# Performance work log

Measured on AMD Instinct MI355X. Metric: run time of the kernel, lower is better.

The kernel has to match this reference:

```python
import jax, jax.numpy as jnp
import numpy as np

# Mamba3/SSD selective state-space mixer (scalar-A-per-head SSD recurrence,
# causal depthwise conv on x/B/C, gated RMSNorm, in/out projections).
D_MODEL = 1024
EXPAND = 2
D_INNER = EXPAND * D_MODEL            # 2048
HEADDIM = D_MODEL // 16               # 64  (head_count=16 -> headdim 64)
NHEADS = D_INNER // HEADDIM           # 32
D_STATE = 128
CONV_W = 4
CONV_DIM = D_INNER + 2 * D_STATE      # x, B, C share the conv
D_IN_PROJ = 2 * D_INNER + 2 * D_STATE + NHEADS  # z, x, B, C, dt
EPS = 1e-5


def setup_inputs() -> dict:
    key = jax.random.key(0)
    ks = jax.random.split(key, 8)
    B, L = 4, 2048
    hidden = jax.random.normal(ks[0], (B, L, D_MODEL), dtype=jnp.float32)
    W_in = jax.random.normal(ks[1], (D_MODEL, D_IN_PROJ), dtype=jnp.float32) * 0.02
    conv_w = jax.random.normal(ks[2], (CONV_DIM, CONV_W), dtype=jnp.float32) * 0.2
    conv_b = jnp.zeros((CONV_DIM,), dtype=jnp.float32)
    # dt_bias: inverse-softplus of dt ~ U[1e-3, 0.1]
    dt = jnp.exp(jax.random.uniform(ks[3], (NHEADS,)) * (np.log(0.1) - np.log(1e-3)) + np.log(1e-3))
    dt_bias = dt + jnp.log(-jnp.expm1(-dt))
    A_log = jnp.log(jax.random.uniform(ks[4], (NHEADS,), minval=1.0, maxval=16.0))
    D = jnp.ones((NHEADS,), dtype=jnp.float32)
    norm_w = jnp.ones((D_INNER,), dtype=jnp.float32)
    W_out = jax.random.normal(ks[5], (D_INNER, D_MODEL), dtype=jnp.float32) * 0.02
    return {"hidden": hidden, "W_in": W_in, "conv_w": conv_w, "conv_b": conv_b,
            "dt_bias": dt_bias, "A_log": A_log, "D": D, "norm_w": norm_w, "W_out": W_out}


def _silu(x):
    return x * jax.nn.sigmoid(x)


def _mixer(hidden, W_in, conv_w, conv_b, dt_bias, A_log, D, norm_w, W_out):
    Bsz, L, _ = hidden.shape
    zxbcdt = hidden @ W_in                                    # [B,L,D_IN_PROJ]
    z = zxbcdt[..., :D_INNER]
    xBC = zxbcdt[..., D_INNER:D_INNER + CONV_DIM]
    dt = zxbcdt[..., -NHEADS:]                                # [B,L,H]
    # causal depthwise conv, width 4 (small fixed loop over taps)
    xp = jnp.pad(xBC, ((0, 0), (CONV_W - 1, 0), (0, 0)))
    conv = sum(xp[:, k:k + L, :] * conv_w[:, k] for k in range(CONV_W))
    xBC = _silu(conv + conv_b)
    x = xBC[..., :D_INNER].reshape(Bsz, L, NHEADS, HEADDIM)   # [B,L,H,P]
    Bm = xBC[..., D_INNER:D_INNER + D_STATE]                  # [B,L,N]
    Cm = xBC[..., D_INNER + D_STATE:]                         # [B,L,N]
    dt = jax.nn.softplus(dt + dt_bias)                        # [B,L,H]
    dA = jnp.exp(dt * (-jnp.exp(A_log)))                      # [B,L,H] decay in (0,1)
    dBx = jnp.einsum('blh,bln,blhp->blhpn', dt, Bm, x)        # [B,L,H,P,N]

    def step(h, inp):
        dA_t, dBx_t, C_t = inp                                # [B,H],[B,H,P,N],[B,N]
        h = dA_t[:, :, None, None] * h + dBx_t
        y = jnp.einsum('bhpn,bn->bhp', h, C_t)
        return h, y

    h0 = jnp.zeros((Bsz, NHEADS, HEADDIM, D_STATE), dtype=hidden.dtype)
    xs = (jnp.moveaxis(dA, 1, 0), jnp.moveaxis(dBx, 1, 0), jnp.moveaxis(Cm, 1, 0))
    _, ys = jax.lax.scan(step, h0, xs)                        # [L,B,H,P]
    y = jnp.moveaxis(ys, 0, 1) + D[None, None, :, None] * x   # skip term
    y = y.reshape(Bsz, L, D_INNER)
    # gated RMSNorm: norm(y * silu(z))
    y = y * _silu(z)
    y = y * jax.lax.rsqrt(jnp.mean(y * y, axis=-1, keepdims=True) + EPS) * norm_w
    return y @ W_out


def reference(hidden, W_in, conv_w, conv_b, dt_bias, A_log, D, norm_w, W_out):
    return _mixer(hidden, W_in, conv_w, conv_b, dt_bias, A_log, D, norm_w, W_out)
```

## Files before the change

### kernel.cpp

```cpp
#include <hip/hip_runtime.h>
#include <math.h>

#define BSZ 4
#define LEN 2048
#define DM 1024
#define DI 2048
#define HD 64
#define NH 32
#define DS 128
#define CD 2304
#define DP 4384
#define NTOK (BSZ*LEN)
#define QCH 128
#define NCH (LEN/QCH)
#define TOFF (DP-NH)

#define CONV_R 64
#define NRB (NTOK/CONV_R)
#define NPAD 4352

typedef unsigned short ushort_t;
typedef __bf16 bf16x8 __attribute__((ext_vector_type(8)));
typedef ushort_t us8 __attribute__((ext_vector_type(8)));
typedef float f32x4 __attribute__((ext_vector_type(4)));

__device__ __forceinline__ ushort_t f2bf(float f) {
    unsigned u = __float_as_uint(f);
    unsigned r = (u + 0x7FFFu + ((u >> 16) & 1u)) >> 16;
    return (ushort_t)r;
}
__device__ __forceinline__ float bf2f(ushort_t u) {
    return __uint_as_float(((unsigned)u) << 16);
}
__device__ __forceinline__ bf16x8 us2bf(us8 v) {
    union { us8 u; bf16x8 b; } x; x.u = v; return x.b;
}

__device__ __forceinline__ void gl_lds16(const void* g, void* l) {
    __builtin_amdgcn_global_load_lds(
        (const __attribute__((address_space(1))) void*)g,
        (__attribute__((address_space(3))) void*)l, 16, 0, 0);
}

__global__ __launch_bounds__(256) void cvt_bf16(
    const float* __restrict__ A, ushort_t* __restrict__ Ab)
{
    size_t i = ((size_t)blockIdx.x * 256 + threadIdx.x) * 4;
    float4 v = *(const float4*)(A + i);
    ushort_t o[4] = { f2bf(v.x), f2bf(v.y), f2bf(v.z), f2bf(v.w) };
    *(uint2*)(Ab + i) = *(uint2*)o;
}

__global__ __launch_bounds__(256) void transpose_cvt(
    const float* __restrict__ W, ushort_t* __restrict__ Wt,
    const float* __restrict__ colscale, int K, int N, int ldw)
{
    __shared__ float T[32][33];
    const int n0 = blockIdx.x * 32;
    const int k0 = blockIdx.y * 32;
    const int tid = threadIdx.x;
    #pragma unroll
    for (int l = 0; l < 4; l++) {
        int idx = tid + l * 256;
        int ki = idx >> 5, nj = idx & 31;
        int n = n0 + nj;
        float s = colscale ? colscale[k0 + ki] : 1.f;
        T[ki][nj] = (n < N) ? W[(size_t)(k0 + ki) * ldw + n] * s : 0.f;
    }
    __syncthreads();
    #pragma unroll
    for (int l = 0; l < 4; l++) {
        int idx = tid + l * 256;
        int nj = idx >> 5, ki = idx & 31;
        Wt[(size_t)(n0 + nj) * K + k0 + ki] = f2bf(T[ki][nj]);
    }
}

template <bool OB>
__global__ __launch_bounds__(256) void gemm128(
    const ushort_t* __restrict__ A, const ushort_t* __restrict__ Bt,
    void* __restrict__ Cp, const float* __restrict__ rowscale,
    int K, int lda, int ldb, int ldc)
{
    __shared__ __align__(16) ushort_t LA[2][128 * 64];
    __shared__ __align__(16) ushort_t LB[2][128 * 64];
    const int tid = threadIdx.x;
    int bid = blockIdx.y * gridDim.x + blockIdx.x;
    const int nwg = gridDim.x * gridDim.y;
    if (!(nwg & 7)) bid = (bid & 7) * (nwg >> 3) + (bid >> 3);
    const int n0 = (bid % gridDim.x) * 128;
    const int m0 = (bid / gridDim.x) * 128;
    const int lane = tid & 63;
    const int w = tid >> 6;
    const int wm = w >> 1, wn = w & 1;
    const int lm = lane & 15, quad = lane >> 4;
    const int swz = (lm & 7) << 4;
    const int ck0 = ((0 * 64 + quad * 16) ^ swz) >> 1;
    const int ck1 = ((1 * 64 + quad * 16) ^ swz) >> 1;

    const int srow = tid >> 3;
    const int scolb = ((tid & 7) * 16) ^ ((srow & 7) << 4);
    const char* gA = (const char*)A + ((size_t)(m0 + srow) * lda) * 2 + scolb;
    const char* gB = (const char*)Bt + ((size_t)(n0 + srow) * ldb) * 2 + scolb;
    const size_t strA = (size_t)32 * lda * 2;
    const size_t strB = (size_t)32 * ldb * 2;
    const int ldst = tid * 8;

    f32x4 acc[4][4];
    #pragma unroll
    for (int i = 0; i < 4; i++)
        #pragma unroll
        for (int j = 0; j < 4; j++) acc[i][j] = (f32x4){0.f, 0.f, 0.f, 0.f};

    const int NTt = K >> 6;

    auto STAGE = [&](int kt1, int nxt) {
        const char* a = gA + (size_t)kt1 * 128;
        const char* b = gB + (size_t)kt1 * 128;
        #pragma unroll
        for (int j = 0; j < 4; j++)
            gl_lds16(a + j * strA, &LA[nxt][j * 2048 + ldst]);
        #pragma unroll
        for (int j = 0; j < 4; j++)
            gl_lds16(b + j * strB, &LB[nxt][j * 2048 + ldst]);
    };

    STAGE(0, 0);

    for (int kt = 0; kt < NTt; ++kt) {
        const int cur = kt & 1;
        __builtin_amdgcn_s_barrier();
        if (kt + 1 < NTt) {
            STAGE(kt + 1, cur ^ 1);
            asm volatile("s_waitcnt vmcnt(8)" ::: "memory");
        } else {
            asm volatile("s_waitcnt vmcnt(0)" ::: "memory");
        }
        __builtin_amdgcn_s_barrier();

        bf16x8 af[4][2], bf[4][2];
        #pragma unroll
        for (int s = 0; s < 4; s++) {
            const int rb = (wm * 64 + s * 16 + lm) << 6;
            af[s][0] = *(const bf16x8*)&LA[cur][rb + ck0];
            af[s][1] = *(const bf16x8*)&LA[cur][rb + ck1];
        }
        #pragma unroll
        for (int t = 0; t < 4; t++) {
            const int rb = (wn * 64 + t * 16 + lm) << 6;
            bf[t][0] = *(const bf16x8*)&LB[cur][rb + ck0];
            bf[t][1] = *(const bf16x8*)&LB[cur][rb + ck1];
        }
        __builtin_amdgcn_s_setprio(1);
        #pragma unroll
        for (int kk = 0; kk < 2; kk++)
            #pragma unroll
            for (int s = 0; s < 4; s++)
                #pragma unroll
                for (int t = 0; t < 4; t++)
                    acc[s][t] = __builtin_amdgcn_mfma_f32_16x16x32_bf16(
                        af[s][kk], bf[t][kk], acc[s][t], 0, 0, 0);
        __builtin_amdgcn_s_setprio(0);
    }

    #pragma unroll
    for (int s = 0; s < 4; s++) {
        const int row = m0 + wm * 64 + s * 16 + quad * 4;
        float rs[4] = {1.f, 1.f, 1.f, 1.f};
        if (!OB && rowscale) {
            #pragma unroll
            for (int r = 0; r < 4; r++) rs[r] = rowscale[row + r];
        }
        #pragma unroll
        for (int t = 0; t < 4; t++) {
            const int col = n0 + wn * 64 + t * 16 + lm;
            #pragma unroll
            for (int r = 0; r < 4; r++) {
                if (OB)
                    ((ushort_t*)Cp)[(size_t)(row + r) * ldc + col] = f2bf(acc[s][t][r]);
                else
                    ((float*)Cp)[(size_t)(row + r) * ldc + col] = acc[s][t][r] * rs[r];
            }
        }
    }
}

__global__ __launch_bounds__(256) void conv_silu_bf16(
    const ushort_t* __restrict__ xbcb, const float* __restrict__ cw,
    const float* __restrict__ cb, ushort_t* __restrict__ xT,
    ushort_t* __restrict__ Bn, ushort_t* __restrict__ BT,
    ushort_t* __restrict__ Cn)
{
    __shared__ ushort_t Tl[256][68];
    const int tid = threadIdx.x;
    const int c = blockIdx.x * 256 + tid;
    const int rb = blockIdx.y;
    const int row0 = rb * CONV_R;
    const bool isBC = (blockIdx.x == 8);

    const float w0 = cw[c*4+0], w1 = cw[c*4+1], w2 = cw[c*4+2], w3 = cw[c*4+3];
    const float bias = cb[c];
    float h0 = 0.f, h1 = 0.f, h2 = 0.f;
    if ((row0 & (LEN - 1)) != 0) {
        h0 = bf2f(xbcb[(size_t)(row0 - 3) * NPAD + c]);
        h1 = bf2f(xbcb[(size_t)(row0 - 2) * NPAD + c]);
        h2 = bf2f(xbcb[(size_t)(row0 - 1) * NPAD + c]);
    }
    const ushort_t* p = xbcb + (size_t)row0 * NPAD + c;
    for (int r = 0; r < CONV_R; r++) {
        float xin = bf2f(*p);
        float a = bias + w0*h0 + w1*h1 + w2*h2 + w3*xin;
        ushort_t bv = f2bf(a / (1.f + __expf(-a)));
        Tl[tid][r] = bv;
        if (isBC) {
            int row = row0 + r;
            if (tid < DS) Bn[(size_t)row * DS + tid] = bv;
            else          Cn[(size_t)row * DS + (tid - DS)] = bv;
        }
        h0 = h1; h1 = h2; h2 = xin;
        p += NPAD;
    }
    __syncthreads();

    const int seg = tid & 7;
    const int clb = tid >> 3;
    if (!isBC) {
        #pragma unroll
        for (int pass = 0; pass < 8; pass++) {
            int cl = pass * 32 + clb;
            int cc = blockIdx.x * 256 + cl;
            us8 v;
            #pragma unroll
            for (int j = 0; j < 8; j++) v[j] = Tl[cl][seg * 8 + j];
            *(us8*)&xT[(size_t)cc * NTOK + row0 + seg * 8] = v;
        }
    } else {
        #pragma unroll
        for (int pass = 0; pass < 4; pass++) {
            int n = pass * 32 + clb;
            us8 v;
            #pragma unroll
            for (int j = 0; j < 8; j++) v[j] = Tl[n][seg * 8 + j];
            *(us8*)&BT[(size_t)n * NTOK + row0 + seg * 8] = v;
        }
    }
}

__global__ __launch_bounds__(256) void gct_gemm(
    const ushort_t* __restrict__ Bn, const ushort_t* __restrict__ Cn,
    float* __restrict__ Graw)
{
    const int bc = blockIdx.x;
    const int chunk = bc % NCH;
    const int b = bc / NCH;
    const size_t rowbase = (size_t)b * LEN + (size_t)chunk * QCH;
    const int tid = threadIdx.x;
    const int w = tid >> 6, lane = tid & 63;
    const int lm = lane & 15, quad = lane >> 4;
    const int tw0 = w * 32;

    f32x4 acc[2][8];
    #pragma unroll
    for (int ti = 0; ti < 2; ti++)
        #pragma unroll
        for (int sj = 0; sj < 8; sj++) acc[ti][sj] = (f32x4){0.f, 0.f, 0.f, 0.f};

    #pragma unroll
    for (int ks = 0; ks < 4; ks++) {
        const int k0 = ks * 32 + quad * 8;
        bf16x8 a0 = *(const bf16x8*)&Cn[(rowbase + tw0 + lm) * DS + k0];
        bf16x8 a1 = *(const bf16x8*)&Cn[(rowbase + tw0 + 16 + lm) * DS + k0];
        #pragma unroll
        for (int sj = 0; sj < 8; sj++) {
            bf16x8 bb = *(const bf16x8*)&Bn[(rowbase + sj * 16 + lm) * DS + k0];
            acc[0][sj] = __builtin_amdgcn_mfma_f32_16x16x32_bf16(a0, bb, acc[0][sj], 0, 0, 0);
            acc[1][sj] = __builtin_amdgcn_mfma_f32_16x16x32_bf16(a1, bb, acc[1][sj], 0, 0, 0);
        }
    }
    float* G = Graw + (size_t)bc * (QCH * QCH);
    #pragma unroll
    for (int ti = 0; ti < 2; ti++)
        #pragma unroll
        for (int sj = 0; sj < 8; sj++)
            #pragma unroll
            for (int r = 0; r < 4; r++)
                G[(size_t)(tw0 + ti * 16 + quad * 4 + r) * QCH + sj * 16 + lm] = acc[ti][sj][r];
}

__global__ __launch_bounds__(256) void dt_proc_fp32(
    const float* __restrict__ hidden, const float* __restrict__ W_in,
    const float* __restrict__ dt_bias, const float* __restrict__ A_log,
    float* __restrict__ dtv, float* __restrict__ ldA)
{
    const int h = threadIdx.x & 31;
    const int tt = threadIdx.x >> 5;
    const int t = blockIdx.x * 8 + tt;
    const float* hr = hidden + (size_t)t * DM;
    const float* wc = W_in + TOFF + h;
    float a0 = 0.f, a1 = 0.f, a2 = 0.f, a3 = 0.f;
    for (int k = 0; k < DM; k += 4) {
        a0 += hr[k+0] * wc[(size_t)(k+0) * DP];
        a1 += hr[k+1] * wc[(size_t)(k+1) * DP];
        a2 += hr[k+2] * wc[(size_t)(k+2) * DP];
        a3 += hr[k+3] * wc[(size_t)(k+3) * DP];
    }
    float v = (a0 + a1) + (a2 + a3) + dt_bias[h];
    float sp = (v > 20.f) ? v : log1pf(expf(v));
    int idx = t * NH + h;
    dtv[idx] = sp;
    ldA[idx] = -sp * expf(A_log[h]);
}

__global__ __launch_bounds__(64) void scan_chunk(
    const float* __restrict__ dtv, const float* __restrict__ ldA,
    float* __restrict__ lcpb, float* __restrict__ dtsb,
    float* __restrict__ coefb, float* __restrict__ csum)
{
    const int blk = blockIdx.x;
    const int chunk = blk % NCH;
    const int bh = blk / NCH;
    const int h = bh % NH;
    const int b = bh / NH;
    const int lane = threadIdx.x;
    const size_t rowbase = (size_t)b * LEN + (size_t)chunk * QCH;
    const int t0 = 2 * lane, t1 = 2 * lane + 1;
    float v0 = ldA[(rowbase + t0) * NH + h];
    float v1 = ldA[(rowbase + t1) * NH + h];
    float d0 = dtv[(rowbase + t0) * NH + h];
    float d1 = dtv[(rowbase + t1) * NH + h];
    float pair = v0 + v1;
    #pragma unroll
    for (int off = 1; off < 64; off <<= 1) {
        float n = __shfl_up(pair, off, 64);
        if (lane >= off) pair += n;
    }
    float l1 = pair, l0 = pair - v1;
    float total = __shfl(pair, 63, 64);
    size_t base = (size_t)blk * QCH;
    *(float2*)&lcpb[base + t0] = make_float2(l0, l1);
    *(float2*)&dtsb[base + t0] = make_float2(d0, d1);
    *(float2*)&coefb[base + t0] =
        make_float2(__expf(total - l0) * d0, __expf(total - l1) * d1);
    if (lane == 63) csum[blk] = total;
}

__global__ __launch_bounds__(256) void phase1_mfma(
    const ushort_t* __restrict__ xT, const ushort_t* __restrict__ BT,
    const float* __restrict__ coefb, float* __restrict__ S)
{
    const int h = blockIdx.x & (NH - 1);
    const int bc = blockIdx.x >> 5;
    const int chunk = bc % NCH;
    const int b = bc / NCH;
    const int blko = (b * NH + h) * NCH + chunk;
    const int tid = threadIdx.x;
    const size_t rowbase = (size_t)b * LEN + (size_t)chunk * QCH;

    __shared__ float coef[QCH];
    if (tid < QCH) coef[tid] = coefb[(size_t)blko * QCH + tid];
    __syncthreads();

    const int w = tid >> 6, lane = tid & 63;
    const int lm = lane & 15, quad = lane >> 4;
    const int nw0 = w * 32;

    f32x4 acc[4][2];
    #pragma unroll
    for (int i = 0; i < 4; i++)
        #pragma unroll
        for (int j = 0; j < 2; j++) acc[i][j] = (f32x4){0.f, 0.f, 0.f, 0.f};

    #pragma unroll
    for (int ks = 0; ks < 4; ks++) {
        const int k0 = ks * 32 + quad * 8;
        bf16x8 a[4];
        #pragma unroll
        for (int mi = 0; mi < 4; mi++)
            a[mi] = *(const bf16x8*)&xT[(size_t)(h * HD + mi * 16 + lm) * NTOK + rowbase + k0];
        float cf[8];
        #pragma unroll
        for (int j = 0; j < 8; j++) cf[j] = coef[k0 + j];
        #pragma unroll
        for (int ni = 0; ni < 2; ni++) {
            us8 raw = *(const us8*)&BT[(size_t)(nw0 + ni * 16 + lm) * NTOK + rowbase + k0];
            us8 sb;
            #pragma unroll
            for (int j = 0; j < 8; j++) sb[j] = f2bf(bf2f(raw[j]) * cf[j]);
            bf16x8 bfr = us2bf(sb);
            __builtin_amdgcn_s_setprio(1);
            #pragma unroll
            for (int mi = 0; mi < 4; mi++)
                acc[mi][ni] = __builtin_amdgcn_mfma_f32_16x16x32_bf16(a[mi], bfr, acc[mi][ni], 0, 0, 0);
            __builtin_amdgcn_s_setprio(0);
        }
    }
    float* Sb = S + (size_t)blko * (HD * DS);
    #pragma unroll
    for (int mi = 0; mi < 4; mi++)
        #pragma unroll
        for (int ni = 0; ni < 2; ni++)
            #pragma unroll
            for (int r = 0; r < 4; r++)
                Sb[(size_t)(mi * 16 + quad * 4 + r) * DS + nw0 + ni * 16 + lm] = acc[mi][ni][r];
}

__global__ __launch_bounds__(256) void phase2(
    const float* __restrict__ S, const float* __restrict__ csum,
    ushort_t* __restrict__ hsb)
{
    const int bh = blockIdx.x >> 3;
    const int esl = blockIdx.x & 7;
    const int tid = threadIdx.x;
    const int eb = esl * 1024 + tid;
    float run[4] = {0.f, 0.f, 0.f, 0.f};
    for (int c = 0; c < NCH; c++) {
        float P = __expf(csum[bh * NCH + c]);
        size_t base = (size_t)(bh * NCH + c) * (HD * DS);
        #pragma unroll
        for (int i = 0; i < 4; i++) {
            size_t idx = base + eb + i * 256;
            float s = S[idx];
            hsb[idx] = f2bf(run[i]);
            run[i] = P * run[i] + s;
        }
    }
}

__global__ __launch_bounds__(256) void phase3_mfma(
    const ushort_t* __restrict__ xT, const ushort_t* __restrict__ Cn,
    const ushort_t* __restrict__ hsb, const float* __restrict__ Graw,
    const float* __restrict__ lcpb, const float* __restrict__ dtsb,
    const float* __restrict__ Dvec, ushort_t* __restrict__ zxb,
    float* __restrict__ ss)
{
    const int tid = threadIdx.x;
    const int h = blockIdx.x & (NH - 1);
    const int bc = blockIdx.x >> 5;
    const int chunk = bc % NCH;
    const int b = bc / NCH;
    const int blko = (b * NH + h) * NCH + chunk;
    const size_t rowbase = (size_t)b * LEN + (size_t)chunk * QCH;

    __shared__ float lcp[QCH];
    __shared__ float dts[QCH];
    if (tid < QCH) {
        lcp[tid] = lcpb[(size_t)blko * QCH + tid];
        dts[tid] = dtsb[(size_t)blko * QCH + tid];
    }
    __syncthreads();

    const int w = tid >> 6, lane = tid & 63;
    const int lm = lane & 15, quad = lane >> 4;
    const int tw0 = w * 32;

    const float* Gr = Graw + (size_t)bc * (QCH * QCH);
    const ushort_t* hsp = hsb + (size_t)blko * (HD * DS);

    f32x4 acc2[2][4];
    #pragma unroll
    for (int ti = 0; ti < 2; ti++)
        #pragma unroll
        for (int pi = 0; pi < 4; pi++) acc2[ti][pi] = (f32x4){0.f, 0.f, 0.f, 0.f};

    #pragma unroll
    for (int ks = 0; ks < 8; ks++) {
        bf16x8 a[2], bb[4];
        if (ks < 4) {
            const int k0 = ks * 32 + quad * 8;
            #pragma unroll
            for (int ti = 0; ti < 2; ti++) {
                int t = tw0 + ti * 16 + lm;
                float lt = lcp[t];
                const float* gp = Gr + (size_t)t * QCH + k0;
                float4 g0 = *(const float4*)gp;
                float4 g1 = *(const float4*)(gp + 4);
                float ge[8] = { g0.x, g0.y, g0.z, g0.w, g1.x, g1.y, g1.z, g1.w };
                us8 sb;
                #pragma unroll
                for (int j = 0; j < 8; j++) {
                    int s = k0 + j;
                    float wv = (s <= t) ? (__expf(lt - lcp[s]) * dts[s]) : 0.f;
                    sb[j] = f2bf(ge[j] * wv);
                }
                a[ti] = us2bf(sb);
            }
            #pragma unroll
            for (int pi = 0; pi < 4; pi++)
                bb[pi] = *(const bf16x8*)&xT[(size_t)(h * HD + pi * 16 + lm) * NTOK + rowbase + k0];
        } else {
            const int k0 = (ks - 4) * 32 + quad * 8;
            #pragma unroll
            for (int ti = 0; ti < 2; ti++) {
                int t = tw0 + ti * 16 + lm;
                float sc = __expf(lcp[t]);
                us8 raw = *(const us8*)&Cn[(rowbase + t) * DS + k0];
                us8 sb;
                #pragma unroll
                for (int j = 0; j < 8; j++) sb[j] = f2bf(bf2f(raw[j]) * sc);
                a[ti] = us2bf(sb);
            }
            #pragma unroll
            for (int pi = 0; pi < 4; pi++)
                bb[pi] = *(const bf16x8*)&hsp[(size_t)(pi * 16 + lm) * DS + k0];
        }
        __builtin_amdgcn_s_setprio(1);
        #pragma unroll
        for (int ti = 0; ti < 2; ti++)
            #pragma unroll
            for (int pi = 0; pi < 4; pi++)
                acc2[ti][pi] = __builtin_amdgcn_mfma_f32_16x16x32_bf16(a[ti], bb[pi], acc2[ti][pi], 0, 0, 0);
        __builtin_amdgcn_s_setprio(0);
    }

    const float Dh = Dvec[h];
    float vsq[2][4] = {};
    #pragma unroll
    for (int ti = 0; ti < 2; ti++)
        #pragma unroll
        for (int pi = 0; pi < 4; pi++) {
            int tb = tw0 + ti * 16 + quad * 4;
            int col = h * HD + pi * 16 + lm;
            ushort4 xv = *(const ushort4*)&xT[(size_t)(h * HD + pi * 16 + lm) * NTOK + rowbase + tb];
            const ushort_t* xe = (const ushort_t*)&xv;
            #pragma unroll
            for (int r = 0; r < 4; r++) {
                size_t grow = rowbase + tb + r;
                float y = acc2[ti][pi][r] + Dh * bf2f(xe[r]);
                float z = bf2f(zxb[grow * NPAD + col]);
                float v = y * (z / (1.f + __expf(-z)));
                vsq[ti][r] += v * v;
                zxb[grow * NPAD + DI + col] = f2bf(v);
            }
        }
    #pragma unroll
    for (int ti = 0; ti < 2; ti++)
        #pragma unroll
        for (int r = 0; r < 4; r++) {
            float s = vsq[ti][r];
            s += __shfl_xor(s, 1, 64);
            s += __shfl_xor(s, 2, 64);
            s += __shfl_xor(s, 4, 64);
            s += __shfl_xor(s, 8, 64);
            if (lm == 0) {
                int tb = tw0 + ti * 16 + quad * 4 + r;
                atomicAdd(&ss[rowbase + tb], s);
            }
        }
}

__global__ __launch_bounds__(256) void rms_finalize(
    const float* __restrict__ ss, float* __restrict__ rr)
{
    int t = blockIdx.x * 256 + threadIdx.x;
    rr[t] = rsqrtf(ss[t] * (1.f / DI) + 1e-5f);
}

extern "C" void kernel_launch(void* const* d_in, const int* in_sizes, int n_in,
                              void* d_out, int out_size, void* d_ws, size_t ws_size,
                              hipStream_t stream)
{
    const float* hidden  = (const float*)d_in[0];
    const float* W_in    = (const float*)d_in[1];
    const float* conv_w  = (const float*)d_in[2];
    const float* conv_b  = (const float*)d_in[3];
    const float* dt_bias = (const float*)d_in[4];
    const float* A_log   = (const float*)d_in[5];
    const float* Dv      = (const float*)d_in[6];
    const float* norm_w  = (const float*)d_in[7];
    const float* W_out   = (const float*)d_in[8];
    float* out = (float*)d_out;

    char* ws = (char*)d_ws;
    size_t o = 0;
    ushort_t* zxb  = (ushort_t*)(ws + o); o += (size_t)NTOK * NPAD * 2;
    float* S       = (float*)(ws + o);    o += (size_t)BSZ * NH * NCH * HD * DS * 4;
    ushort_t* xT   = (ushort_t*)(ws + o); o += (size_t)DI * NTOK * 2;
    ushort_t* Bn   = (ushort_t*)(ws + o); o += (size_t)NTOK * DS * 2;
    ushort_t* BT   = (ushort_t*)(ws + o); o += (size_t)DS * NTOK * 2;
    ushort_t* Cn   = (ushort_t*)(ws + o); o += (size_t)NTOK * DS * 2;
    ushort_t* hsb  = (ushort_t*)(ws + o); o += (size_t)BSZ * NH * NCH * HD * DS * 2;
    float* Graw    = (float*)(ws + o);    o += (size_t)BSZ * NCH * QCH * QCH * 4;
    float* dtv     = (float*)(ws + o);    o += (size_t)NTOK * NH * 4;
    float* ldA     = (float*)(ws + o);    o += (size_t)NTOK * NH * 4;
    float* lcpb    = (float*)(ws + o);    o += (size_t)BSZ * NH * LEN * 4;
    float* dtsb    = (float*)(ws + o);    o += (size_t)BSZ * NH * LEN * 4;
    float* coefb   = (float*)(ws + o);    o += (size_t)BSZ * NH * LEN * 4;
    float* csum    = (float*)(ws + o);    o += (size_t)BSZ * NH * NCH * 4;
    float* ss      = (float*)(ws + o);    o += (size_t)NTOK * 4;
    float* rr      = (float*)(ws + o);    o += (size_t)NTOK * 4;
    ushort_t* Ah   = (ushort_t*)S;
    ushort_t* W1t  = (ushort_t*)((char*)S + (size_t)NTOK * DM * 2);
    ushort_t* Wot  = hsb;
    ushort_t* xbcb = zxb + DI;
    ushort_t* ynb  = zxb + DI;

    hipMemsetAsync(ss, 0, (size_t)NTOK * 4, stream);
    cvt_bf16<<<(NTOK * DM) / 1024, 256, 0, stream>>>(hidden, Ah);
    transpose_cvt<<<dim3(NPAD / 32, DM / 32), 256, 0, stream>>>(
        W_in, W1t, nullptr, DM, NPAD, DP);
    gemm128<true><<<dim3(NPAD / 128, NTOK / 128), 256, 0, stream>>>(
        Ah, W1t, zxb, nullptr, DM, DM, DM, NPAD);
    conv_silu_bf16<<<dim3(CD / 256, NRB), 256, 0, stream>>>(
        xbcb, conv_w, conv_b, xT, Bn, BT, Cn);
    gct_gemm<<<BSZ * NCH, 256, 0, stream>>>(Bn, Cn, Graw);
    dt_proc_fp32<<<NTOK / 8, 256, 0, stream>>>(hidden, W_in, dt_bias, A_log, dtv, ldA);
    scan_chunk<<<BSZ * NH * NCH, 64, 0, stream>>>(dtv, ldA, lcpb, dtsb, coefb, csum);
    phase1_mfma<<<BSZ * NH * NCH, 256, 0, stream>>>(xT, BT, coefb, S);
    phase2<<<BSZ * NH * 8, 256, 0, stream>>>(S, csum, hsb);
    phase3_mfma<<<BSZ * NH * NCH, 256, 0, stream>>>(
        xT, Cn, hsb, Graw, lcpb, dtsb, Dv, zxb, ss);
    rms_finalize<<<NTOK / 256, 256, 0, stream>>>(ss, rr);
    transpose_cvt<<<dim3(DM / 32, DI / 32), 256, 0, stream>>>(
        W_out, Wot, norm_w, DI, DM, DM);
    gemm128<false><<<dim3(DM / 128, NTOK / 128), 256, 0, stream>>>(
        ynb, Wot, out, rr, DI, NPAD, DI, DM);
}
```

Before: 507.2 us.

## Use triple-buffered K=32 GEMM for input projection and fold RMS finalize into output GEMM

Adds a new input-projection GEMM kernel that stages K tiles of 32 into three LDS buffers, prefetching two tiles ahead with explicit vmcnt waits. Its smaller LDS footprint lets launch bounds request three workgroups per CU, aiming for better latency hiding and occupancy. Separately, the rms_finalize kernel is dropped and the rsqrt is computed in the output GEMM epilogue directly from the sum-of-squares buffer, removing one launch and one small buffer. The trade-off is more barriers per K step and a slightly heavier epilogue.

```diff
diff --git a/kernel.cpp b/kernel.cpp
--- a/kernel.cpp
+++ b/kernel.cpp
@@ -73,6 +73,100 @@
         int idx = tid + l * 256;
         int nj = idx >> 5, ki = idx & 31;
         Wt[(size_t)(n0 + nj) * K + k0 + ki] = f2bf(T[ki][nj]);
+    }
+}
+
+__global__ __launch_bounds__(256, 3) void gemm1_tb(
+    const ushort_t* __restrict__ A, const ushort_t* __restrict__ Bt,
+    ushort_t* __restrict__ C, int K, int lda, int ldb, int ldc)
+{
+    __shared__ __align__(16) ushort_t LA[3][128 * 32];
+    __shared__ __align__(16) ushort_t LB[3][128 * 32];
+    const int tid = threadIdx.x;
+    int bid = blockIdx.y * gridDim.x + blockIdx.x;
+    const int nwg = gridDim.x * gridDim.y;
+    if (!(nwg & 7)) bid = (bid & 7) * (nwg >> 3) + (bid >> 3);
+    const int n0 = (bid % gridDim.x) * 128;
+    const int m0 = (bid / gridDim.x) * 128;
+    const int lane = tid & 63;
+    const int w = tid >> 6;
+    const int wm = w >> 1, wn = w & 1;
+    const int lm = lane & 15, quad = lane >> 4;
+    const int ck = ((quad * 16) ^ (((lm >> 1) & 3) << 4)) >> 1;
+
+    const int srow = tid >> 2;
+    const int scolb = ((tid & 3) * 16) ^ (((tid >> 3) & 3) << 4);
+    const char* gA = (const char*)A + ((size_t)(m0 + srow) * lda) * 2 + scolb;
+    const char* gB = (const char*)Bt + ((size_t)(n0 + srow) * ldb) * 2 + scolb;
+    const size_t strA = (size_t)64 * lda * 2;
+    const size_t strB = (size_t)64 * ldb * 2;
+    const int ldst = tid * 8;
+
+    f32x4 acc[4][4];
+    #pragma unroll
+    for (int i = 0; i < 4; i++)
+        #pragma unroll
+        for (int j = 0; j < 4; j++) acc[i][j] = (f32x4){0.f, 0.f, 0.f, 0.f};
+
+    const int NTt = K >> 5;
+
+    auto STAGE = [&](int kt1, int buf) {
+        const char* a = gA + (size_t)kt1 * 64;
+        const char* b = gB + (size_t)kt1 * 64;
+        gl_lds16(a + 0 * strA, &LA[buf][0 * 2048 + ldst]);
+        gl_lds16(a + 1 * strA, &LA[buf][1 * 2048 + ldst]);
+        gl_lds16(b + 0 * strB, &LB[buf][0 * 2048 + ldst]);
+        gl_lds16(b + 1 * strB, &LB[buf][1 * 2048 + ldst]);
+    };
+
+    STAGE(0, 0);
+    STAGE(1, 1);
+
+    int cur = 0;
+    int sb  = 2;
+    for (int kt = 0; kt < NTt; ++kt) {
+        __builtin_amdgcn_s_barrier();
+        const int ahead = NTt - 1 - kt;
+        if (ahead >= 2) {
+            STAGE(kt + 2, sb);
+            asm volatile("s_waitcnt vmcnt(8)" ::: "memory");
+        } else if (ahead == 1) {
+            asm volatile("s_waitcnt vmcnt(4)" ::: "memory");
+        } else {
+            asm volatile("s_waitcnt vmcnt(0)" ::: "memory");
+        }
+        __builtin_amdgcn_s_barrier();
+
+        bf16x8 af[4], bf[4];
+        #pragma unroll
+        for (int s = 0; s < 4; s++)
+            af[s] = *(const bf16x8*)&LA[cur][((wm * 64 + s * 16 + lm) << 5) + ck];
+        #pragma unroll
+        for (int t = 0; t < 4; t++)
+            bf[t] = *(const bf16x8*)&LB[cur][((wn * 64 + t * 16 + lm) << 5) + ck];
+        __builtin_amdgcn_s_setprio(1);
+        #pragma unroll
+        for (int s = 0; s < 4; s++)
+            #pragma unroll
+            for (int t = 0; t < 4; t++)
+                acc[s][t] = __builtin_amdgcn_mfma_f32_16x16x32_bf16(
+                    af[s], bf[t], acc[s][t], 0, 0, 0);
+        __builtin_amdgcn_s_setprio(0);
+
+        cur = (cur == 2) ? 0 : cur + 1;
+        sb  = (sb == 2) ? 0 : sb + 1;
+    }
+
+    #pragma unroll
+    for (int s = 0; s < 4; s++) {
+        const int row = m0 + wm * 64 + s * 16 + quad * 4;
+        #pragma unroll
+        for (int t = 0; t < 4; t++) {
+            const int col = n0 + wn * 64 + t * 16 + lm;
+            #pragma unroll
+            for (int r = 0; r < 4; r++)
+                C[(size_t)(row + r) * ldc + col] = f2bf(acc[s][t][r]);
+        }
     }
 }
 
@@ -169,7 +263,8 @@
         float rs[4] = {1.f, 1.f, 1.f, 1.f};
         if (!OB && rowscale) {
             #pragma unroll
-            for (int r = 0; r < 4; r++) rs[r] = rowscale[row + r];
+            for (int r = 0; r < 4; r++)
+                rs[r] = rsqrtf(rowscale[row + r] * (1.f / DI) + 1e-5f);
         }
         #pragma unroll
         for (int t = 0; t < 4; t++) {
@@ -546,13 +641,6 @@
                 atomicAdd(&ss[rowbase + tb], s);
             }
         }
-}
-
-__global__ __launch_bounds__(256) void rms_finalize(
-    const float* __restrict__ ss, float* __restrict__ rr)
-{
-    int t = blockIdx.x * 256 + threadIdx.x;
-    rr[t] = rsqrtf(ss[t] * (1.f / DI) + 1e-5f);
 }
 
 extern "C" void kernel_launch(void* const* d_in, const int* in_sizes, int n_in,
@@ -587,7 +675,6 @@
     float* coefb   = (float*)(ws + o);    o += (size_t)BSZ * NH * LEN * 4;
     float* csum    = (float*)(ws + o);    o += (size_t)BSZ * NH * NCH * 4;
     float* ss      = (float*)(ws + o);    o += (size_t)NTOK * 4;
-    float* rr      = (float*)(ws + o);    o += (size_t)NTOK * 4;
     ushort_t* Ah   = (ushort_t*)S;
     ushort_t* W1t  = (ushort_t*)((char*)S + (size_t)NTOK * DM * 2);
     ushort_t* Wot  = hsb;
@@ -598,8 +685,8 @@
     cvt_bf16<<<(NTOK * DM) / 1024, 256, 0, stream>>>(hidden, Ah);
     transpose_cvt<<<dim3(NPAD / 32, DM / 32), 256, 0, stream>>>(
         W_in, W1t, nullptr, DM, NPAD, DP);
-    gemm128<true><<<dim3(NPAD / 128, NTOK / 128), 256, 0, stream>>>(
-        Ah, W1t, zxb, nullptr, DM, DM, DM, NPAD);
+    gemm1_tb<<<dim3(NPAD / 128, NTOK / 128), 256, 0, stream>>>(
+        Ah, W1t, zxb, DM, DM, DM, NPAD);
     conv_silu_bf16<<<dim3(CD / 256, NRB), 256, 0, stream>>>(
         xbcb, conv_w, conv_b, xT, Bn, BT, Cn);
     gct_gemm<<<BSZ * NCH, 256, 0, stream>>>(Bn, Cn, Graw);
@@ -609,9 +696,8 @@
     phase2<<<BSZ * NH * 8, 256, 0, stream>>>(S, csum, hsb);
     phase3_mfma<<<BSZ * NH * NCH, 256, 0, stream>>>(
         xT, Cn, hsb, Graw, lcpb, dtsb, Dv, zxb, ss);
-    rms_finalize<<<NTOK / 256, 256, 0, stream>>>(ss, rr);
     transpose_cvt<<<dim3(DM / 32, DI / 32), 256, 0, stream>>>(
         W_out, Wot, norm_w, DI, DM, DM);
     gemm128<false><<<dim3(DM / 128, NTOK / 128), 256, 0, stream>>>(
-        ynb, Wot, out, rr, DI, NPAD, DI, DM);
-}
+        ynb, Wot, out, ss, DI, NPAD, DI, DM);
+}
```

Measured after the change: 498.1 us. About the same (-1.8%).
